# Performance work log

Measured on AMD Instinct MI355X. Metric: run time of the kernel, lower is better.

## Reference

```python
import jax, jax.numpy as jnp
import numpy as np

C = 64
CQ = C // 8


def setup_inputs() -> dict:
    key = jax.random.key(0)
    ks = jax.random.split(key, 8)
    x = jax.random.normal(ks[0], (8, C, 64, 64), dtype=jnp.float32)
    s = 1.0 / np.sqrt(C)
    Wq = jax.random.normal(ks[1], (CQ, C), dtype=jnp.float32) * s
    bq = jax.random.normal(ks[2], (CQ,), dtype=jnp.float32) * s
    Wk = jax.random.normal(ks[3], (CQ, C), dtype=jnp.float32) * s
    bk = jax.random.normal(ks[4], (CQ,), dtype=jnp.float32) * s
    Wv = jax.random.normal(ks[5], (C, C), dtype=jnp.float32) * s
    bv = jax.random.normal(ks[6], (C,), dtype=jnp.float32) * s
    gamma = jnp.array([0.5], dtype=jnp.float32)  # nonzero so value path contributes
    return {"x": x, "Wq": Wq, "bq": bq, "Wk": Wk, "bk": bk, "Wv": Wv, "bv": bv, "gamma": gamma}


def reference(x, Wq, bq, Wk, bk, Wv, bv, gamma):
    B, Cc, H, W = x.shape
    xf = x.reshape(B, Cc, H * W)  # [B, C, N]
    # 1x1 conv == channel-mixing linear
    f = jnp.einsum('oc,bcn->bon', Wq, xf) + bq[None, :, None]  # [B, C/8, N]
    g = jnp.einsum('oc,bcn->bon', Wk, xf) + bk[None, :, None]  # [B, C/8, N]
    h = jnp.einsum('oc,bcn->bon', Wv, xf) + bv[None, :, None]  # [B, C, N]
    # scores[b,i,j] = f[b,:,i] . g[b,:,j]; softmax over dim=1 (query dim i)
    scores = jnp.einsum('bdi,bdj->bij', f, g)  # [B, N, N]
    beta = jax.nn.softmax(scores, axis=1)
    o = gamma[0] * jnp.einsum('bcn,bnm->bcm', h, beta) + xf
    return o.reshape(B, Cc, H, W)
```

## Files before the change

kernel.cpp:

```cpp
#include <hip/hip_runtime.h>
#include <hip/hip_fp16.h>


typedef _Float16 half8_t __attribute__((ext_vector_type(8)));
typedef _Float16 half4_t __attribute__((ext_vector_type(4)));
typedef _Float16 half2_t __attribute__((ext_vector_type(2)));
typedef __fp16  fp16x2  __attribute__((ext_vector_type(2)));
typedef float float4_t __attribute__((ext_vector_type(4)));

#define NTOK 4096
#define PRH 72
#define LOG2E 1.44269504088896340736f

#if __has_builtin(__builtin_amdgcn_exp2f)
__device__ __forceinline__ float fexp2(float x) { return __builtin_amdgcn_exp2f(x); }
#else
__device__ __forceinline__ float fexp2(float x) { return exp2f(x); }
#endif

__device__ __forceinline__ half2_t pkcvt(float a, float b) {
    fp16x2 v = __builtin_amdgcn_cvt_pkrtz(a, b);
    return __builtin_bit_cast(half2_t, v);
}

__global__ __launch_bounds__(320) void proj_kernel(
    const float* __restrict__ x,
    const float* __restrict__ Wq, const float* __restrict__ bq,
    const float* __restrict__ Wk, const float* __restrict__ bk,
    const float* __restrict__ Wv, const float* __restrict__ bv,
    __half* __restrict__ fTR, __half* __restrict__ gT16, __half* __restrict__ hM)
{
    __shared__ __align__(16) _Float16 xh[32 * PRH];
    const int t      = threadIdx.x;
    const int blk    = blockIdx.x;
    const int b      = blockIdx.y;
    const int n0     = blk * 32;
    const int kt64   = blk >> 1;
    const int t4base = (blk & 1) * 2;

    if (t < 256) {
#pragma unroll
        for (int i = 0; i < 2; i++) {
            const int idx = t + i * 256;
            const int c = idx >> 3, f4 = idx & 7;
            float4 v = *(const float4*)(x + (((size_t)(b * 64 + c)) << 12) + n0 + f4 * 4);
            const int cs = c ^ ((f4 & 3) << 4);
            xh[(f4 * 4 + 0) * PRH + cs] = (_Float16)v.x;
            xh[(f4 * 4 + 1) * PRH + cs] = (_Float16)v.y;
            xh[(f4 * 4 + 2) * PRH + cs] = (_Float16)v.z;
            xh[(f4 * 4 + 3) * PRH + cs] = (_Float16)v.w;
        }
    }

    const int w    = t >> 6;
    const int lane = t & 63;
    const int q    = lane >> 4;
    const int ml   = lane & 15;

    const float* wrow;
    if (w == 0) wrow = (ml < 8) ? (Wq + ml * 64) : (Wk + (ml - 8) * 64);
    else        wrow = Wv + ((w - 1) * 16 + ml) * 64;
    half4_t afr[4];
#pragma unroll
    for (int ks = 0; ks < 4; ks++) {
        float4 wv4 = *(const float4*)(wrow + ks * 16 + q * 4);
        afr[ks] = (half4_t){(_Float16)wv4.x, (_Float16)wv4.y,
                            (_Float16)wv4.z, (_Float16)wv4.w};
    }
    float4 bias4;
    if (w == 0) bias4 = (q < 2) ? *(const float4*)(bq + q * 4)
                                : *(const float4*)(bk + (q - 2) * 4);
    else        bias4 = *(const float4*)(bv + (w - 1) * 16 + q * 4);

    __syncthreads();

#pragma unroll
    for (int cg = 0; cg < 2; cg++) {
        const int tok  = cg * 16 + ml;
        const int swz  = (tok >> 2) & 3;
        float4_t acc = (float4_t){0.f, 0.f, 0.f, 0.f};
#pragma unroll
        for (int ks = 0; ks < 4; ks++) {
            half4_t bfr = *(const half4_t*)(&xh[tok * PRH + ((ks ^ swz) * 16 + q * 4)]);
            acc = __builtin_amdgcn_mfma_f32_16x16x16f16(afr[ks], bfr, acc, 0, 0, 0);
        }
        acc[0] += bias4.x; acc[1] += bias4.y; acc[2] += bias4.z; acc[3] += bias4.w;
        const int gtok = n0 + tok;
        const int t4   = t4base + cg;

        if (w == 0) {
            __half* rec = fTR + ((size_t)b << 16) + (size_t)(kt64 * 16 + ml) * 64;
            if (q < 2) {
                half4_t fv = {(_Float16)(acc[0] * LOG2E), (_Float16)(acc[1] * LOG2E),
                              (_Float16)(acc[2] * LOG2E), (_Float16)(acc[3] * LOG2E)};
                *(half4_t*)(rec + q * 16 + t4 * 4) = fv;
            } else {
                half4_t cv = (half4_t){};
                if (q == 2) cv[0] = (_Float16)1.0f;
                *(half4_t*)(rec + q * 16 + t4 * 4) = cv;
            }
            float gn2p = acc[0] * acc[0] + acc[1] * acc[1] +
                         acc[2] * acc[2] + acc[3] * acc[3];
            float gn2 = gn2p + __shfl_xor(gn2p, 16, 64);
            if (q >= 2) {
                half4_t gv = {(_Float16)acc[0], (_Float16)acc[1],
                              (_Float16)acc[2], (_Float16)acc[3]};
                __half* gp = gT16 + (size_t)((b << 12) + gtok) * 16;
                *(half4_t*)(gp + (q - 2) * 4) = gv;
                if (q == 2) {
                    const float M = (LOG2E * 4.6f) * __builtin_sqrtf(gn2) + 1.0f;
                    *(half4_t*)(gp + 8) = (half4_t){(_Float16)(-M), 0, 0, 0};
                } else {
                    *(half4_t*)(gp + 12) = (half4_t){};
                }
            }
        } else {
            const int ch = (w - 1) * 16 + q * 4;
#pragma unroll
            for (int r = 0; r < 4; r++)
                hM[(((size_t)b * 64 + ch + r) << 12) + gtok] = __float2half(acc[r]);
        }
    }
}

#define PAIR(SEA, SOA, SEB, SOB, OFF)                                           \
    {                                                                           \
        float eA0 = fexp2(SEA[0]), eA1 = fexp2(SEA[1]),                         \
              eA2 = fexp2(SEA[2]), eA3 = fexp2(SEA[3]);                         \
        float oA0 = fexp2(SOA[0]), oA1 = fexp2(SOA[1]),                         \
              oA2 = fexp2(SOA[2]), oA3 = fexp2(SOA[3]);                         \
        float eB0 = fexp2(SEB[0]), eB1 = fexp2(SEB[1]),                         \
              eB2 = fexp2(SEB[2]), eB3 = fexp2(SEB[3]);                         \
        float oB0 = fexp2(SOB[0]), oB1 = fexp2(SOB[1]),                         \
              oB2 = fexp2(SOB[2]), oB3 = fexp2(SOB[3]);                         \
        half2_t eaA = pkcvt(eA0, eA1), ebA = pkcvt(eA2, eA3);                   \
        half2_t oaA = pkcvt(oA0, oA1), obA = pkcvt(oA2, oA3);                   \
        half2_t eaB = pkcvt(eB0, eB1), ebB = pkcvt(eB2, eB3);                   \
        half2_t oaB = pkcvt(oB0, oB1), obB = pkcvt(oB2, oB3);                   \
        half8_t pA8 = {eaA[0], eaA[1], ebA[0], ebA[1],                          \
                       oaA[0], oaA[1], obA[0], obA[1]};                         \
        half8_t pB8 = {eaB[0], eaB[1], ebB[0], ebB[1],                          \
                       oaB[0], oaB[1], obB[0], obB[1]};                         \
        __builtin_amdgcn_s_setprio(1);                                          \
        accLA = __builtin_amdgcn_mfma_f32_16x16x32_f16(ones8, pA8, accLA, 0, 0, 0); \
        accLB = __builtin_amdgcn_mfma_f32_16x16x32_f16(ones8, pB8, accLB, 0, 0, 0); \
        _Pragma("unroll")                                                       \
        for (int cg = 0; cg < 4; cg++) {                                        \
            half4_t ahE = *(const half4_t*)(hbL + cg * (16 * PRH) + (OFF));     \
            half4_t ahO = *(const half4_t*)(hbL + cg * (16 * PRH) + (OFF) + 16);\
            half8_t ah8 = {ahE[0], ahE[1], ahE[2], ahE[3],                      \
                           ahO[0], ahO[1], ahO[2], ahO[3]};                     \
            accA[cg] = __builtin_amdgcn_mfma_f32_16x16x32_f16(ah8, pA8, accA[cg], 0, 0, 0); \
            accB[cg] = __builtin_amdgcn_mfma_f32_16x16x32_f16(ah8, pB8, accB[cg], 0, 0, 0); \
        }                                                                       \
        __builtin_amdgcn_s_setprio(0);                                          \
    }

template<int NT>
__global__ __launch_bounds__(256) void attn_kernel(
    const __half* __restrict__ fTR, const __half* __restrict__ gT16,
    const __half* __restrict__ hM,
    __half* __restrict__ Pacc, float* __restrict__ Lsum)
{
    __shared__ __align__(16) _Float16 hl[2][64 * PRH];
    const int tid   = threadIdx.x;
    const int w     = tid >> 6;
    const int lane  = tid & 63;
    const int q     = lane >> 4;
    const int ml    = lane & 15;
    const int b     = blockIdx.y;
    const int split = blockIdx.z;
    const int colA  = blockIdx.x * 128 + w * 16 + ml;
    const int colB  = colA + 64;

    half4_t gfA = *(const half4_t*)(gT16 + ((size_t)((b << 12) + colA)) * 16 + q * 4);
    half4_t gfB = *(const half4_t*)(gT16 + ((size_t)((b << 12) + colB)) * 16 + q * 4);

    float4_t accA[4], accB[4];
#pragma unroll
    for (int cg = 0; cg < 4; cg++) {
        accA[cg] = (float4_t){0.f, 0.f, 0.f, 0.f};
        accB[cg] = (float4_t){0.f, 0.f, 0.f, 0.f};
    }
    float4_t accLA = (float4_t){0.f, 0.f, 0.f, 0.f};
    float4_t accLB = (float4_t){0.f, 0.f, 0.f, 0.f};
    const half8_t ones8 = {(_Float16)1.0f, (_Float16)1.0f, (_Float16)1.0f,
                           (_Float16)1.0f, (_Float16)1.0f, (_Float16)1.0f,
                           (_Float16)1.0f, (_Float16)1.0f};

    const int kt0 = split * NT;
    const int c0  = tid >> 3;
    const int g0  = tid & 7;

    const __half* srow0 = hM + ((size_t)(b * 64 + c0) << 12) + kt0 * 64 + g0 * 8;
    const __half* srow1 = srow0 + ((size_t)32 << 12);
    const __half* fptr  = fTR + ((size_t)b << 16) + (size_t)(kt0 * 16 + ml) * 64 + q * 16;

    uint4 s0 = *(const uint4*)srow0;
    uint4 s1 = *(const uint4*)srow1;
    half8_t f01 = *(const half8_t*)fptr;
    half8_t f23 = *(const half8_t*)(fptr + 8);
    *(uint4*)(&hl[0][c0 * PRH + g0 * 8])        = s0;
    *(uint4*)(&hl[0][(c0 + 32) * PRH + g0 * 8]) = s1;
    __syncthreads();

#pragma unroll 1
    for (int kt = 0; kt < NT; kt++) {
        const _Float16* hbL = &hl[kt & 1][ml * PRH + q * 4];
        half4_t afn0 = __builtin_shufflevector(f01, f01, 0, 1, 2, 3);
        half4_t afn1 = __builtin_shufflevector(f01, f01, 4, 5, 6, 7);
        half4_t afn2 = __builtin_shufflevector(f23, f23, 0, 1, 2, 3);
        half4_t afn3 = __builtin_shufflevector(f23, f23, 4, 5, 6, 7);

        __builtin_amdgcn_s_setprio(1);
        float4_t stA0 = __builtin_amdgcn_mfma_f32_16x16x16f16(
            afn0, gfA, (float4_t){0.f, 0.f, 0.f, 0.f}, 0, 0, 0);
        float4_t stA1 = __builtin_amdgcn_mfma_f32_16x16x16f16(
            afn1, gfA, (float4_t){0.f, 0.f, 0.f, 0.f}, 0, 0, 0);
        float4_t stA2 = __builtin_amdgcn_mfma_f32_16x16x16f16(
            afn2, gfA, (float4_t){0.f, 0.f, 0.f, 0.f}, 0, 0, 0);
        float4_t stA3 = __builtin_amdgcn_mfma_f32_16x16x16f16(
            afn3, gfA, (float4_t){0.f, 0.f, 0.f, 0.f}, 0, 0, 0);
        float4_t stB0 = __builtin_amdgcn_mfma_f32_16x16x16f16(
            afn0, gfB, (float4_t){0.f, 0.f, 0.f, 0.f}, 0, 0, 0);
        float4_t stB1 = __builtin_amdgcn_mfma_f32_16x16x16f16(
            afn1, gfB, (float4_t){0.f, 0.f, 0.f, 0.f}, 0, 0, 0);
        float4_t stB2 = __builtin_amdgcn_mfma_f32_16x16x16f16(
            afn2, gfB, (float4_t){0.f, 0.f, 0.f, 0.f}, 0, 0, 0);
        float4_t stB3 = __builtin_amdgcn_mfma_f32_16x16x16f16(
            afn3, gfB, (float4_t){0.f, 0.f, 0.f, 0.f}, 0, 0, 0);
        __builtin_amdgcn_s_setprio(0);

        if (kt + 1 < NT) {
            f01 = *(const half8_t*)(fptr + 1024);
            f23 = *(const half8_t*)(fptr + 1032);
            s0 = *(const uint4*)(srow0 + 64);
            s1 = *(const uint4*)(srow1 + 64);
            fptr  += 1024;
            srow0 += 64;
            srow1 += 64;
        }

        PAIR(stA0, stA1, stB0, stB1, 0)
        PAIR(stA2, stA3, stB2, stB3, 32)

        if (kt + 1 < NT) {
            _Float16* hn = &hl[(kt + 1) & 1][0];
            *(uint4*)(&hn[c0 * PRH + g0 * 8])        = s0;
            *(uint4*)(&hn[(c0 + 32) * PRH + g0 * 8]) = s1;
        }
        __syncthreads();
    }

    __half* pa = Pacc + (((size_t)(split * 8 + b) * 64) << 12);
#pragma unroll
    for (int cg = 0; cg < 4; cg++)
#pragma unroll
        for (int r = 0; r < 4; r++) {
            int ch = cg * 16 + q * 4 + r;
            pa[((size_t)ch << 12) + colA] = __float2half(accA[cg][r]);
            pa[((size_t)ch << 12) + colB] = __float2half(accB[cg][r]);
        }
    if (q == 0) {
        Lsum[((size_t)(split * 8 + b) << 12) + colA] = accLA[0];
        Lsum[((size_t)(split * 8 + b) << 12) + colB] = accLB[0];
    }
}

template<int S>
__global__ __launch_bounds__(256) void merge_kernel(
    const __half* __restrict__ Pacc, const float* __restrict__ Lsum,
    const float* __restrict__ x, const float* __restrict__ gammap,
    float* __restrict__ out)
{
    __shared__ float invL[64];
    const int tid  = threadIdx.x;
    const int c4   = tid & 15;
    const int chh  = tid >> 4;
    const int b    = blockIdx.y;
    const int col0 = blockIdx.x * 64;
    const int ch   = blockIdx.z * 16 + chh;

    if (tid < 64) {
        float L = 0.f;
#pragma unroll
        for (int s = 0; s < S; s++)
            L += Lsum[((size_t)(s * 8 + b) << 12) + col0 + tid];
        invL[tid] = gammap[0] / L;
    }
    __syncthreads();

    const int cc = c4 * 4;
    const size_t base = (((size_t)b * 64 + ch) << 12) + col0 + cc;
    float4 xv = *(const float4*)(x + base);
    float o0 = 0.f, o1 = 0.f, o2 = 0.f, o3 = 0.f;
#pragma unroll
    for (int s = 0; s < S; s++) {
        half4_t pv = *(const half4_t*)(Pacc +
            (((size_t)(s * 8 + b) * 64 + ch) << 12) + col0 + cc);
        o0 += (float)pv[0];
        o1 += (float)pv[1];
        o2 += (float)pv[2];
        o3 += (float)pv[3];
    }
    float4 ov;
    ov.x = o0 * invL[cc]     + xv.x;
    ov.y = o1 * invL[cc + 1] + xv.y;
    ov.z = o2 * invL[cc + 2] + xv.z;
    ov.w = o3 * invL[cc + 3] + xv.w;
    *(float4*)(out + base) = ov;
}

extern "C" void kernel_launch(void* const* d_in, const int* in_sizes, int n_in,
                              void* d_out, int out_size, void* d_ws, size_t ws_size,
                              hipStream_t stream) {
    const float* x     = (const float*)d_in[0];
    const float* Wq    = (const float*)d_in[1];
    const float* bq    = (const float*)d_in[2];
    const float* Wk    = (const float*)d_in[3];
    const float* bk    = (const float*)d_in[4];
    const float* Wv    = (const float*)d_in[5];
    const float* bv    = (const float*)d_in[6];
    const float* gamma = (const float*)d_in[7];
    float* out = (float*)d_out;

    const size_t fr_bytes  = (size_t)8 * 65536 * 2;
    const size_t g_bytes   = (size_t)8 * NTOK * 16 * 2;
    const size_t hM_bytes  = (size_t)8 * 64 * NTOK * 2;
    const size_t pa_split  = (size_t)8 * 64 * NTOK * 2;
    const size_t l_split   = (size_t)8 * NTOK * sizeof(float);
    const size_t base_need = fr_bytes + g_bytes + hM_bytes;

    int S = 1;
    if (ws_size >= base_need + 8 * (pa_split + l_split)) S = 8;
    else if (ws_size >= base_need + 4 * (pa_split + l_split)) S = 4;
    else if (ws_size >= base_need + 2 * (pa_split + l_split)) S = 2;

    char* p = (char*)d_ws;
    __half* fTR  = (__half*)p;  p += fr_bytes;
    __half* gT16 = (__half*)p;  p += g_bytes;
    __half* hM   = (__half*)p;  p += hM_bytes;
    __half* Pacc = (__half*)p;  p += (size_t)S * pa_split;
    float*  Lsum = (float*)p;

    proj_kernel<<<dim3(128, 8), 320, 0, stream>>>(x, Wq, bq, Wk, bk, Wv, bv,
                                                  fTR, gT16, hM);
    if (S == 8) {
        attn_kernel<8><<<dim3(32, 8, 8), 256, 0, stream>>>(fTR, gT16, hM, Pacc, Lsum);
        merge_kernel<8><<<dim3(64, 8, 4), 256, 0, stream>>>(Pacc, Lsum, x, gamma, out);
    } else if (S == 4) {
        attn_kernel<16><<<dim3(32, 8, 4), 256, 0, stream>>>(fTR, gT16, hM, Pacc, Lsum);
        merge_kernel<4><<<dim3(64, 8, 4), 256, 0, stream>>>(Pacc, Lsum, x, gamma, out);
    } else if (S == 2) {
        attn_kernel<32><<<dim3(32, 8, 2), 256, 0, stream>>>(fTR, gT16, hM, Pacc, Lsum);
        merge_kernel<2><<<dim3(64, 8, 4), 256, 0, stream>>>(Pacc, Lsum, x, gamma, out);
    } else {
        attn_kernel<64><<<dim3(32, 8, 1), 256, 0, stream>>>(fTR, gT16, hM, Pacc, Lsum);
        merge_kernel<1><<<dim3(64, 8, 4), 256, 0, stream>>>(Pacc, Lsum, x, gamma, out);
    }
}
```

Baseline: 123.0 us.

## Load value tiles with global_load_lds into XOR-swizzled LDS

```diff
diff --git a/kernel.cpp b/kernel.cpp
--- a/kernel.cpp
+++ b/kernel.cpp
@@ -22,6 +22,10 @@
     fp16x2 v = __builtin_amdgcn_cvt_pkrtz(a, b);
     return __builtin_bit_cast(half2_t, v);
 }
+
+#define GLDS(G, L) __builtin_amdgcn_global_load_lds(                            \
+    (const __attribute__((address_space(1))) unsigned int*)(G),                 \
+    (__attribute__((address_space(3))) unsigned int*)(L), 16, 0, 0)
 
 __global__ __launch_bounds__(320) void proj_kernel(
     const float* __restrict__ x,
@@ -115,16 +119,23 @@
                 }
             }
         } else {
-            const int ch = (w - 1) * 16 + q * 4;
+            const int ch  = (w - 1) * 16 + q * 4;
+            const int pos = ((t4 >> 1) << 5) + ((ml >> 2) << 3) + ((t4 & 1) << 2) + (ml & 3);
+            const size_t rowbase = ((size_t)(b * 64 + ch) << 12) + (size_t)kt64 * 64 + pos;
 #pragma unroll
             for (int r = 0; r < 4; r++)
-                hM[(((size_t)b * 64 + ch + r) << 12) + gtok] = __float2half(acc[r]);
-        }
-    }
-}
-
-#define PAIR(SEA, SOA, SEB, SOB, OFF)                                           \
+                hM[rowbase + ((size_t)r << 12)] = __float2half(acc[r]);
+        }
+    }
+}
+
+#define PAIR(SEA, SOA, SEB, SOB, GOFF)                                          \
     {                                                                           \
+        const _Float16* hp = hb + (GOFF);                                       \
+        half8_t ah0 = *(const half8_t*)(hp);                                    \
+        half8_t ah1 = *(const half8_t*)(hp + 1024);                             \
+        half8_t ah2 = *(const half8_t*)(hp + 2048);                             \
+        half8_t ah3 = *(const half8_t*)(hp + 3072);                             \
         float eA0 = fexp2(SEA[0]), eA1 = fexp2(SEA[1]),                         \
               eA2 = fexp2(SEA[2]), eA3 = fexp2(SEA[3]);                         \
         float oA0 = fexp2(SOA[0]), oA1 = fexp2(SOA[1]),                         \
@@ -144,15 +155,14 @@
         __builtin_amdgcn_s_setprio(1);                                          \
         accLA = __builtin_amdgcn_mfma_f32_16x16x32_f16(ones8, pA8, accLA, 0, 0, 0); \
         accLB = __builtin_amdgcn_mfma_f32_16x16x32_f16(ones8, pB8, accLB, 0, 0, 0); \
-        _Pragma("unroll")                                                       \
-        for (int cg = 0; cg < 4; cg++) {                                        \
-            half4_t ahE = *(const half4_t*)(hbL + cg * (16 * PRH) + (OFF));     \
-            half4_t ahO = *(const half4_t*)(hbL + cg * (16 * PRH) + (OFF) + 16);\
-            half8_t ah8 = {ahE[0], ahE[1], ahE[2], ahE[3],                      \
-                           ahO[0], ahO[1], ahO[2], ahO[3]};                     \
-            accA[cg] = __builtin_amdgcn_mfma_f32_16x16x32_f16(ah8, pA8, accA[cg], 0, 0, 0); \
-            accB[cg] = __builtin_amdgcn_mfma_f32_16x16x32_f16(ah8, pB8, accB[cg], 0, 0, 0); \
-        }                                                                       \
+        accA[0] = __builtin_amdgcn_mfma_f32_16x16x32_f16(ah0, pA8, accA[0], 0, 0, 0); \
+        accB[0] = __builtin_amdgcn_mfma_f32_16x16x32_f16(ah0, pB8, accB[0], 0, 0, 0); \
+        accA[1] = __builtin_amdgcn_mfma_f32_16x16x32_f16(ah1, pA8, accA[1], 0, 0, 0); \
+        accB[1] = __builtin_amdgcn_mfma_f32_16x16x32_f16(ah1, pB8, accB[1], 0, 0, 0); \
+        accA[2] = __builtin_amdgcn_mfma_f32_16x16x32_f16(ah2, pA8, accA[2], 0, 0, 0); \
+        accB[2] = __builtin_amdgcn_mfma_f32_16x16x32_f16(ah2, pB8, accB[2], 0, 0, 0); \
+        accA[3] = __builtin_amdgcn_mfma_f32_16x16x32_f16(ah3, pA8, accA[3], 0, 0, 0); \
+        accB[3] = __builtin_amdgcn_mfma_f32_16x16x32_f16(ah3, pB8, accB[3], 0, 0, 0); \
         __builtin_amdgcn_s_setprio(0);                                          \
     }
 
@@ -162,12 +172,13 @@
     const __half* __restrict__ hM,
     __half* __restrict__ Pacc, float* __restrict__ Lsum)
 {
-    __shared__ __align__(16) _Float16 hl[2][64 * PRH];
+    __shared__ __align__(16) _Float16 hl[2][4096];
     const int tid   = threadIdx.x;
     const int w     = tid >> 6;
     const int lane  = tid & 63;
     const int q     = lane >> 4;
     const int ml    = lane & 15;
+    const int m7    = ml & 7;
     const int b     = blockIdx.y;
     const int split = blockIdx.z;
     const int colA  = blockIdx.x * 128 + w * 16 + ml;
@@ -189,24 +200,31 @@
                            (_Float16)1.0f, (_Float16)1.0f};
 
     const int kt0 = split * NT;
-    const int c0  = tid >> 3;
-    const int g0  = tid & 7;
-
-    const __half* srow0 = hM + ((size_t)(b * 64 + c0) << 12) + kt0 * 64 + g0 * 8;
-    const __half* srow1 = srow0 + ((size_t)32 << 12);
-    const __half* fptr  = fTR + ((size_t)b << 16) + (size_t)(kt0 * 16 + ml) * 64 + q * 16;
-
-    uint4 s0 = *(const uint4*)srow0;
-    uint4 s1 = *(const uint4*)srow1;
+
+    const int ch0  = tid >> 3;
+    const int gsw  = (tid & 7) ^ (ch0 & 7);
+    const __half* hs0 = hM + ((size_t)(b * 64 + ch0) << 12) + (size_t)kt0 * 64 + gsw * 8;
+    const __half* hs1 = hs0 + ((size_t)32 << 12);
+    const __half* fptr = fTR + ((size_t)b << 16) + (size_t)(kt0 * 16 + ml) * 64 + q * 16;
+
+    const int gx0 = ((q ^ m7) << 3);
+    const int gx1 = (((4 + q) ^ m7) << 3);
+
+    GLDS(hs0, &hl[0][tid * 8]);
+    GLDS(hs1, &hl[0][2048 + tid * 8]);
     half8_t f01 = *(const half8_t*)fptr;
     half8_t f23 = *(const half8_t*)(fptr + 8);
-    *(uint4*)(&hl[0][c0 * PRH + g0 * 8])        = s0;
-    *(uint4*)(&hl[0][(c0 + 32) * PRH + g0 * 8]) = s1;
     __syncthreads();
 
 #pragma unroll 1
     for (int kt = 0; kt < NT; kt++) {
-        const _Float16* hbL = &hl[kt & 1][ml * PRH + q * 4];
+        if (kt + 1 < NT) {
+            _Float16* nb = &hl[(kt + 1) & 1][0];
+            GLDS(hs0 + (kt + 1) * 64, nb + tid * 8);
+            GLDS(hs1 + (kt + 1) * 64, nb + 2048 + tid * 8);
+        }
+
+        const _Float16* hb = &hl[kt & 1][ml << 6];
         half4_t afn0 = __builtin_shufflevector(f01, f01, 0, 1, 2, 3);
         half4_t afn1 = __builtin_shufflevector(f01, f01, 4, 5, 6, 7);
         half4_t afn2 = __builtin_shufflevector(f23, f23, 0, 1, 2, 3);
@@ -234,21 +252,12 @@
         if (kt + 1 < NT) {
             f01 = *(const half8_t*)(fptr + 1024);
             f23 = *(const half8_t*)(fptr + 1032);
-            s0 = *(const uint4*)(srow0 + 64);
-            s1 = *(const uint4*)(srow1 + 64);
-            fptr  += 1024;
-            srow0 += 64;
-            srow1 += 64;
-        }
-
-        PAIR(stA0, stA1, stB0, stB1, 0)
-        PAIR(stA2, stA3, stB2, stB3, 32)
-
-        if (kt + 1 < NT) {
-            _Float16* hn = &hl[(kt + 1) & 1][0];
-            *(uint4*)(&hn[c0 * PRH + g0 * 8])        = s0;
-            *(uint4*)(&hn[(c0 + 32) * PRH + g0 * 8]) = s1;
-        }
+            fptr += 1024;
+        }
+
+        PAIR(stA0, stA1, stB0, stB1, gx0)
+        PAIR(stA2, stA3, stB2, stB3, gx1)
+
         __syncthreads();
     }
 
```

New measurement: 119.7 us. -2.7%, faster.
